# Performance work log

Hardware: AMD Instinct MI355X
Metric: run time of the kernel (lower is better)

The kernel has to match this reference:

```python
import jax, jax.numpy as jnp
import numpy as np

B, CIN, COUT, H, W = 16, 96, 96, 96, 96
K = 3   # hidden_kernels (conv), odd -> same padding
A = 3   # attn_kernels, odd -> stride-1 unfold preserves H*W positions


def _conv(x, w, p):
    # NCHW conv with symmetric padding p, stride 1, no bias
    return jax.lax.conv_general_dilated(
        x, w, window_strides=(1, 1), padding=[(p, p), (p, p)],
        dimension_numbers=("NCHW", "OIHW", "NCHW"))


def _unfold_nonoverlap(y, a):
    # torch nn.Unfold(a, stride=a): [B,C,H,W] -> [B, C*a*a, L], channel-major (c,kh,kw)
    b, c, h, w = y.shape
    hb, wb = h // a, w // a
    y = y.reshape(b, c, hb, a, wb, a).transpose(0, 1, 3, 5, 2, 4)
    return y.reshape(b, c * a * a, hb * wb)


def _unfold_stride1(y, a):
    # torch nn.Unfold(a, padding=a//2): [B,C,H,W] -> [B, C*a*a, H*W]
    b, c, h, w = y.shape
    p = a // 2
    yp = jnp.pad(y, ((0, 0), (0, 0), (p, p), (p, p)))
    # small fixed a*a loop (9 shifts), channel-major (c,kh,kw) ordering
    patches = jnp.stack([yp[:, :, i:i + h, j:j + w]
                         for i in range(a) for j in range(a)], axis=2)
    return patches.reshape(b, c * a * a, h * w)


def setup_inputs() -> dict:
    key = jax.random.key(0)
    kx, k1, k2, k3 = jax.random.split(key, 4)
    x = jax.random.normal(kx, (B, CIN, H, W), dtype=jnp.float32)
    W1 = jax.random.normal(k1, (COUT, CIN, K, K), dtype=jnp.float32) * 0.05
    W2 = jax.random.normal(k2, (COUT, CIN, K, K), dtype=jnp.float32) * 0.05
    W3 = jax.random.normal(k3, (COUT, CIN, K, K), dtype=jnp.float32) * 0.05
    return {"x": x, "W1": W1, "W2": W2, "W3": W3}


def reference(x, W1, W2, W3):
    a, c, p = A, COUT, K // 2
    b = x.shape[0]
    y1 = _unfold_nonoverlap(_conv(x, W1, p), a)   # [B, C*a^2, L]
    y2 = _unfold_nonoverlap(_conv(x, W2, p), a)   # [B, C*a^2, L]
    L = y1.shape[-1]
    y1 = y1.reshape(b, c, a * a, L).transpose(0, 2, 1, 3)  # [B, a^2, C, L]
    y2 = y2.reshape(b, c, a * a, L).transpose(0, 2, 3, 1)  # [B, a^2, L, C]
    attn = jnp.einsum("bkcl,bkld->bkcd", y1, y2)           # [B, a^2, C, C]
    # torch: transpose(1,3).flatten(2) -> [B, C, C*a^2], then scale + softmax(dim=2)
    attn = attn.transpose(0, 3, 2, 1).reshape(b, c, c * a * a)
    attn = jax.nn.softmax(attn / np.float32(np.sqrt(c * a * a)), axis=2)
    v = _unfold_stride1(_conv(x, W3, p), a)        # [B, C*a^2, H*W]
    out = jnp.einsum("bcm,bml->bcl", attn, v)      # [B, C, H*W]
    return out.reshape(b, c, H, W)
```

## Files before the change

kernel.cpp:

```cpp
#include <hip/hip_runtime.h>
#include <math.h>
#include <stdint.h>

constexpr int BB  = 16;
constexpr int CH  = 96;
constexpr int HH  = 96;
constexpr int WW  = 96;
constexpr int HWI = HH * WW;
constexpr int CHW = CH * HWI;
constexpr int IMG = BB * CHW;
constexpr int ATT = BB * CH * CH * 9;
constexpr int WPK = 27 * 6 * 64 * 8;

typedef short short8 __attribute__((ext_vector_type(8)));
typedef float floatx4 __attribute__((ext_vector_type(4)));

__device__ __forceinline__ ushort f2bf(float f) {
  union { float f; unsigned u; } v; v.f = f;
  unsigned r = (v.u + 0x7fffu + ((v.u >> 16) & 1u)) >> 16;
  return (ushort)r;
}
__device__ __forceinline__ float bf2f(ushort h) {
  union { float f; unsigned u; } v; v.u = ((unsigned)h) << 16;
  return v.f;
}
__device__ __forceinline__ uint packhl(float v) {
  const ushort h = f2bf(v);
  const ushort l = f2bf(v - bf2f(h));
  return (uint)h | ((uint)l << 16);
}

__device__ __forceinline__ void gl_lds_b128(const void* g, void* s) {
  auto gp = (const __attribute__((address_space(1))) void*)(uintptr_t)g;
  auto sp = (__attribute__((address_space(3))) void*)(uintptr_t)s;
  __builtin_amdgcn_global_load_lds(gp, sp, 16, 0, 0);
}

__global__ __launch_bounds__(256) void prepack(
    const float* __restrict__ src, ushort* __restrict__ dst)
{
  const int g = blockIdx.y;
  const int p = blockIdx.x * 256 + threadIdx.x;
  const float* s = src + (size_t)g * WPK;
  ushort* d = dst + (size_t)g * WPK;
  const int j    = p & 7;
  const int lane = (p >> 3) & 63;
  const int rest = p >> 9;
  const int mt = rest % 6;
  const int kc = rest / 6;
  const int m  = mt * 16 + (lane & 15);
  const int k  = kc * 32 + (lane >> 4) * 8 + j;
  const int ci = k % 96;
  const int o  = k / 96;
  d[p] = f2bf(s[m * 864 + ci * 9 + o]);
}

template<bool INBF, bool OUTBF>
__global__ __launch_bounds__(256, 2) void conv_mfma_t(
    const void* __restrict__ Xv, const ushort* __restrict__ Wpk,
    void* __restrict__ Yv, int wbstride)
{
  const int b    = blockIdx.y;
  const int tile = blockIdx.x;
  const int ty0  = (tile / 6) * 12;
  const int tx0  = (tile % 6) * 16;
  const int tid  = threadIdx.x;
  const int lane = tid & 63;
  const int w    = tid >> 6;
  const int nc   = lane & 15;
  const int q    = lane >> 4;

  __shared__ __attribute__((aligned(16))) ushort Xs[252 * 104];
  __shared__ __attribute__((aligned(16))) ushort Wl[2][3072];

  const ushort* wp = Wpk + (size_t)b * wbstride;

  {
    gl_lds_b128(wp + w * 512 + lane * 8,
                (ushort*)Wl[0] + __builtin_amdgcn_readfirstlane(w * 512));
    if (w < 2)
      gl_lds_b128(wp + (w + 4) * 512 + lane * 8,
                  (ushort*)Wl[0] + __builtin_amdgcn_readfirstlane((w + 4) * 512));
  }

  if (tid < 252) {
    const int ly = tid / 18, lx = tid % 18;
    const int gy = ty0 - 1 + ly, gx = tx0 - 1 + lx;
    const bool inb = ((unsigned)gy < 96u) & ((unsigned)gx < 96u);
    ushort* dst = &Xs[tid * 104];
    if constexpr (INBF) {
      const ushort* src = (const ushort*)Xv + (size_t)b * CHW + gy * WW + gx;
#pragma unroll 4
      for (int cg = 0; cg < 24; ++cg) {
        ushort u0 = 0, u1 = 0, u2 = 0, u3 = 0;
        if (inb) {
          const ushort* s = src + (size_t)(cg * 4) * HWI;
          u0 = s[0]; u1 = s[HWI]; u2 = s[2 * HWI]; u3 = s[3 * HWI];
        }
        ushort4 u; u.x = u0; u.y = u1; u.z = u2; u.w = u3;
        *(ushort4*)(dst + cg * 4) = u;
      }
    } else {
      const float* src = (const float*)Xv + (size_t)b * CHW + gy * WW + gx;
#pragma unroll 4
      for (int cg = 0; cg < 24; ++cg) {
        float f0 = 0.f, f1 = 0.f, f2 = 0.f, f3 = 0.f;
        if (inb) {
          const float* s = src + (size_t)(cg * 4) * HWI;
          f0 = s[0]; f1 = s[HWI]; f2 = s[2 * HWI]; f3 = s[3 * HWI];
        }
        ushort4 u;
        u.x = f2bf(f0); u.y = f2bf(f1); u.z = f2bf(f2); u.w = f2bf(f3);
        *(ushort4*)(dst + cg * 4) = u;
      }
    }
  }
  __syncthreads();

  floatx4 acc[6][3];
#pragma unroll
  for (int mt = 0; mt < 6; ++mt)
#pragma unroll
    for (int t = 0; t < 3; ++t)
#pragma unroll
      for (int r = 0; r < 4; ++r) acc[mt][t][r] = 0.f;

  for (int ch = 0; ch < 27; ++ch) {
    if (ch < 26) {
      const ushort* src = wp + (size_t)(ch + 1) * 3072;
      ushort* dstb = (ushort*)Wl[(ch + 1) & 1];
      gl_lds_b128(src + w * 512 + lane * 8,
                  dstb + __builtin_amdgcn_readfirstlane(w * 512));
      if (w < 2)
        gl_lds_b128(src + (w + 4) * 512 + lane * 8,
                    dstb + __builtin_amdgcn_readfirstlane((w + 4) * 512));
    }

    const ushort* wb = Wl[ch & 1];
    const int o  = ch / 3;
    const int cc = ch - o * 3;
    const int dy = o / 3, dx = o - dy * 3;
    const int pc = nc + dx;
    const int cib = cc * 32 + q * 8;

    short8 bfr[3];
#pragma unroll
    for (int t = 0; t < 3; ++t) {
      const int pix = (3 * w + t + dy) * 18 + pc;
      bfr[t] = *(const short8*)(&Xs[pix * 104 + cib]);
    }

#pragma unroll
    for (int mt = 0; mt < 6; ++mt) {
      const short8 af = *(const short8*)(wb + mt * 512 + lane * 8);
#pragma unroll
      for (int t = 0; t < 3; ++t)
        acc[mt][t] = __builtin_amdgcn_mfma_f32_16x16x32_bf16(
            af, bfr[t], acc[mt][t], 0, 0, 0);
    }
    __syncthreads();
  }

#pragma unroll
  for (int mt = 0; mt < 6; ++mt)
#pragma unroll
    for (int t = 0; t < 3; ++t) {
      const int yy = ty0 + 3 * w + t;
      const int xx = tx0 + nc;
#pragma unroll
      for (int r = 0; r < 4; ++r) {
        const int co = mt * 16 + q * 4 + r;
        const size_t off = (size_t)co * HWI + yy * WW + xx;
        if constexpr (OUTBF)
          ((ushort*)Yv + (size_t)b * CHW)[off] = f2bf(acc[mt][t][r]);
        else
          ((float*)Yv + (size_t)b * CHW)[off] = acc[mt][t][r];
      }
    }
}

__global__ __launch_bounds__(256, 2) void conv_dual_mfma(
    const float* __restrict__ X,
    const ushort* __restrict__ WpkA, const ushort* __restrict__ WpkB,
    uint* __restrict__ YA, uint* __restrict__ YB)
{
  const int b    = blockIdx.y;
  const int tile = blockIdx.x;
  const int ty0  = (tile / 6) * 12;
  const int tx0  = (tile % 6) * 16;
  const int tid  = threadIdx.x;
  const int lane = tid & 63;
  const int w    = tid >> 6;
  const int nc   = lane & 15;
  const int q    = lane >> 4;

  __shared__ __attribute__((aligned(16))) ushort Xs[252 * 104];
  __shared__ __attribute__((aligned(16))) ushort Wl[2][6144];

  {
#pragma unroll
    for (int i = 0; i < 3; ++i) {
      const int p  = w + 4 * i;
      const int cv = p / 6;
      const int pt = p - cv * 6;
      const ushort* src = (cv ? WpkB : WpkA) + pt * 512 + lane * 8;
      gl_lds_b128(src, (ushort*)Wl[0] +
                  __builtin_amdgcn_readfirstlane(cv * 3072 + pt * 512));
    }
  }

  if (tid < 252) {
    const int ly = tid / 18, lx = tid % 18;
    const int gy = ty0 - 1 + ly, gx = tx0 - 1 + lx;
    const bool inb = ((unsigned)gy < 96u) & ((unsigned)gx < 96u);
    const float* src = X + (size_t)b * CHW + gy * WW + gx;
    ushort* dst = &Xs[tid * 104];
#pragma unroll 4
    for (int cg = 0; cg < 24; ++cg) {
      float f0 = 0.f, f1 = 0.f, f2 = 0.f, f3 = 0.f;
      if (inb) {
        const float* s = src + (size_t)(cg * 4) * HWI;
        f0 = s[0]; f1 = s[HWI]; f2 = s[2 * HWI]; f3 = s[3 * HWI];
      }
      ushort4 u;
      u.x = f2bf(f0); u.y = f2bf(f1); u.z = f2bf(f2); u.w = f2bf(f3);
      *(ushort4*)(dst + cg * 4) = u;
    }
  }
  __syncthreads();

  floatx4 accA[6][3], accB[6][3];
#pragma unroll
  for (int mt = 0; mt < 6; ++mt)
#pragma unroll
    for (int t = 0; t < 3; ++t)
#pragma unroll
      for (int r = 0; r < 4; ++r) { accA[mt][t][r] = 0.f; accB[mt][t][r] = 0.f; }

  for (int ch = 0; ch < 27; ++ch) {
    if (ch < 26) {
      const size_t coff = (size_t)(ch + 1) * 3072;
      ushort* dstb = (ushort*)Wl[(ch + 1) & 1];
#pragma unroll
      for (int i = 0; i < 3; ++i) {
        const int p  = w + 4 * i;
        const int cv = p / 6;
        const int pt = p - cv * 6;
        const ushort* src = (cv ? WpkB : WpkA) + coff + pt * 512 + lane * 8;
        gl_lds_b128(src, dstb +
                    __builtin_amdgcn_readfirstlane(cv * 3072 + pt * 512));
      }
    }

    const ushort* wb = Wl[ch & 1];
    const int o  = ch / 3;
    const int cc = ch - o * 3;
    const int dy = o / 3, dx = o - dy * 3;
    const int pc = nc + dx;
    const int cib = cc * 32 + q * 8;

    short8 bfr[3];
#pragma unroll
    for (int t = 0; t < 3; ++t) {
      const int pix = (3 * w + t + dy) * 18 + pc;
      bfr[t] = *(const short8*)(&Xs[pix * 104 + cib]);
    }

#pragma unroll
    for (int mt = 0; mt < 6; ++mt) {
      const short8 afA = *(const short8*)(wb + mt * 512 + lane * 8);
#pragma unroll
      for (int t = 0; t < 3; ++t)
        accA[mt][t] = __builtin_amdgcn_mfma_f32_16x16x32_bf16(
            afA, bfr[t], accA[mt][t], 0, 0, 0);
      const short8 afB = *(const short8*)(wb + 3072 + mt * 512 + lane * 8);
#pragma unroll
      for (int t = 0; t < 3; ++t)
        accB[mt][t] = __builtin_amdgcn_mfma_f32_16x16x32_bf16(
            afB, bfr[t], accB[mt][t], 0, 0, 0);
    }
    __syncthreads();
  }

  uint* yA = YA + (size_t)b * CHW;
  uint* yB = YB + (size_t)b * CHW;
#pragma unroll
  for (int mt = 0; mt < 6; ++mt)
#pragma unroll
    for (int t = 0; t < 3; ++t) {
      const int yy = ty0 + 3 * w + t;
      const int xx = tx0 + nc;
#pragma unroll
      for (int r = 0; r < 4; ++r) {
        const int co = mt * 16 + q * 4 + r;
        yA[(size_t)co * HWI + yy * WW + xx] = packhl(accA[mt][t][r]);
        yB[(size_t)co * HWI + yy * WW + xx] = packhl(accB[mt][t][r]);
      }
    }
}

__global__ __launch_bounds__(256) void attn_mfma(
    const uint* __restrict__ Y1, const uint* __restrict__ Y2,
    float* __restrict__ P0, float* __restrict__ P1,
    float* __restrict__ P2, float* __restrict__ P3)
{
  const int bi = blockIdx.x;
  const int b  = bi / 36;
  const int r9 = bi % 36;
  const int k  = r9 >> 2;
  const int qd = r9 & 3;
  const int kh = k / 3, kw = k % 3;
  const int tid  = threadIdx.x;
  const int lane = tid & 63;
  const int wv   = tid >> 6;

  __shared__ ushort Ah[96 * 72], Al[96 * 72], Bh[96 * 72], Bl[96 * 72];

  const uint* y1b = Y1 + (size_t)b * CHW;
  const uint* y2b = Y2 + (size_t)b * CHW;

  const int mg2 = wv >> 1;
  const int ng2 = wv & 1;
  const int cn = lane & 15;
  const int q  = lane >> 4;

  floatx4 acc[3][3];
#pragma unroll
  for (int i = 0; i < 3; ++i)
#pragma unroll
    for (int j = 0; j < 3; ++j)
#pragma unroll
      for (int r = 0; r < 4; ++r) acc[i][j][r] = 0.f;

  const int sj = tid & 31;
  const int sg = tid >> 5;
  const int scol = 3 * sj + kw;

  for (int ss = 0; ss < 4; ++ss) {
    const int s = qd * 4 + ss;
    __syncthreads();
#pragma unroll
    for (int cg = 0; cg < 12; ++cg) {
      const int c = cg * 8 + sg;
      const int cbase = c * 72;
#pragma unroll
      for (int ii = 0; ii < 2; ++ii) {
        const int row = 3 * (s * 2 + ii) + kh;
        const int p   = ii * 32 + sj;
        const size_t goff = (size_t)c * HWI + row * WW + scol;
        const uint u1 = y1b[goff];
        const uint u2 = y2b[goff];
        Ah[cbase + p] = (ushort)(u1 & 0xffffu);
        Al[cbase + p] = (ushort)(u1 >> 16);
        Bh[cbase + p] = (ushort)(u2 & 0xffffu);
        Bl[cbase + p] = (ushort)(u2 >> 16);
      }
    }
    __syncthreads();

#pragma unroll
    for (int kc = 0; kc < 2; ++kc) {
      short8 ah[3], al[3], bh[3], bl[3];
#pragma unroll
      for (int t = 0; t < 3; ++t) {
        const int offA = (mg2 * 48 + t * 16 + cn) * 72 + kc * 32 + q * 8;
        ah[t] = *(const short8*)(&Ah[offA]);
        al[t] = *(const short8*)(&Al[offA]);
        const int offB = (ng2 * 48 + t * 16 + cn) * 72 + kc * 32 + q * 8;
        bh[t] = *(const short8*)(&Bh[offB]);
        bl[t] = *(const short8*)(&Bl[offB]);
      }
#pragma unroll
      for (int i = 0; i < 3; ++i)
#pragma unroll
        for (int j = 0; j < 3; ++j) {
          acc[i][j] = __builtin_amdgcn_mfma_f32_16x16x32_bf16(
              ah[i], bh[j], acc[i][j], 0, 0, 0);
          acc[i][j] = __builtin_amdgcn_mfma_f32_16x16x32_bf16(
              ah[i], bl[j], acc[i][j], 0, 0, 0);
          acc[i][j] = __builtin_amdgcn_mfma_f32_16x16x32_bf16(
              al[i], bh[j], acc[i][j], 0, 0, 0);
        }
    }
  }

  float* P = (qd == 0) ? P0 : (qd == 1) ? P1 : (qd == 2) ? P2 : P3;
#pragma unroll
  for (int i = 0; i < 3; ++i)
#pragma unroll
    for (int j = 0; j < 3; ++j)
#pragma unroll
      for (int r = 0; r < 4; ++r) {
        const int c = mg2 * 48 + i * 16 + q * 4 + r;
        const int d = ng2 * 48 + j * 16 + cn;
        P[((size_t)(b * CH + d) * CH + c) * 9 + k] = acc[i][j][r];
      }
}

__global__ __launch_bounds__(256) void softmax_k(
    const float* __restrict__ P0, const float* __restrict__ P1,
    const float* __restrict__ P2, const float* __restrict__ P3,
    float* __restrict__ attnW)
{
  const int bd = blockIdx.x;
  const size_t base = (size_t)bd * 864;
  float* dst = attnW + base;
  const float rs = 0.0340216824f;
  const int tid = threadIdx.x;

  const size_t i0 = base + tid;
  float v0 = P0[i0] + P1[i0] + P2[i0] + P3[i0];
  float v1 = P0[i0 + 256] + P1[i0 + 256] + P2[i0 + 256] + P3[i0 + 256];
  float v2 = P0[i0 + 512] + P1[i0 + 512] + P2[i0 + 512] + P3[i0 + 512];
  float v3 = (tid < 96)
      ? (P0[i0 + 768] + P1[i0 + 768] + P2[i0 + 768] + P3[i0 + 768])
      : -3.0e38f;

  float mx = fmaxf(fmaxf(v0, v1), fmaxf(v2, v3));

  __shared__ float red[256];
  red[tid] = mx;
  __syncthreads();
#pragma unroll
  for (int s = 128; s > 0; s >>= 1) {
    if (tid < s) red[tid] = fmaxf(red[tid], red[tid + s]);
    __syncthreads();
  }
  mx = red[0];
  __syncthreads();

  const float e0 = expf((v0 - mx) * rs);
  const float e1 = expf((v1 - mx) * rs);
  const float e2 = expf((v2 - mx) * rs);
  const float e3 = (tid < 96) ? expf((v3 - mx) * rs) : 0.f;

  red[tid] = e0 + e1 + e2 + e3;
  __syncthreads();
#pragma unroll
  for (int s = 128; s > 0; s >>= 1) {
    if (tid < s) red[tid] += red[tid + s];
    __syncthreads();
  }
  const float inv = 1.f / red[0];

  dst[tid]       = e0 * inv;
  dst[tid + 256] = e1 * inv;
  dst[tid + 512] = e2 * inv;
  if (tid < 96) dst[tid + 768] = e3 * inv;
}

extern "C" void kernel_launch(void* const* d_in, const int* in_sizes, int n_in,
                              void* d_out, int out_size, void* d_ws, size_t ws_size,
                              hipStream_t stream)
{
  const float* x  = (const float*)d_in[0];
  const float* W1 = (const float*)d_in[1];
  const float* W2 = (const float*)d_in[2];
  const float* W3 = (const float*)d_in[3];

  float* ws    = (float*)d_ws;
  uint*  Y1    = (uint*)ws;
  uint*  Y2    = (uint*)(ws + (size_t)IMG);
  float* attnT = ws + 2 * (size_t)IMG;
  float* attnW = attnT + ATT;
  ushort* pk   = (ushort*)(ws + 2 * (size_t)IMG + 2 * (size_t)ATT);
  ushort* pkW1 = pk;
  ushort* pkW2 = pk + WPK;
  ushort* pkW3 = pk + 2 * (size_t)WPK;
  ushort* pkAW = pk + 3 * (size_t)WPK;
  float* Pd2   = (float*)d_out;
  float* Pd3   = Pd2 + ATT;
  ushort* Y3bf = (ushort*)ws;

  const dim3 cgrid(48, BB);

  prepack  <<<dim3(324, 1),  256, 0, stream>>>(W1, pkW1);
  prepack  <<<dim3(324, 1),  256, 0, stream>>>(W2, pkW2);
  prepack  <<<dim3(324, 1),  256, 0, stream>>>(W3, pkW3);

  conv_dual_mfma<<<cgrid, 256, 0, stream>>>(x, pkW1, pkW2, Y1, Y2);

  attn_mfma<<<BB * 9 * 4, 256, 0, stream>>>(Y1, Y2, attnT, attnW, Pd2, Pd3);
  softmax_k<<<BB * CH, 256, 0, stream>>>(attnT, attnW, Pd2, Pd3, attnW);

  prepack  <<<dim3(324, BB), 256, 0, stream>>>(attnW, pkAW);

  conv_mfma_t<false, true><<<cgrid, 256, 0, stream>>>(x, pkW3, Y3bf, 0);
  conv_mfma_t<true, false><<<cgrid, 256, 0, stream>>>(Y3bf, pkAW, d_out, WPK);
}
```

Baseline: 399.6 us.

## Convert input to channel-last bf16 once and stage weights in large LDS chunks

Adds a pre-pass that casts x to bf16 in pixel-major, channel-contiguous layout, so each conv tile loads its halo with 16-byte vector loads instead of strided scalar fp32 loads. The conv kernel now stages nine weight chunks at a time in LDS (three refills, blocking) instead of double-buffering one chunk per step, which cuts barrier count but raises LDS use and limits occupancy to one block. The fused dual conv is split into two single-conv launches, and the intermediate Y3 is written channel-last for the final conv. The trade-off is an extra cast kernel and extra global traffic for the bf16 copy, lost overlap of weight loads with compute, and re-reading the input for each conv.

```diff
diff --git a/kernel.cpp b/kernel.cpp
--- a/kernel.cpp
+++ b/kernel.cpp
@@ -34,6 +34,33 @@
   auto gp = (const __attribute__((address_space(1))) void*)(uintptr_t)g;
   auto sp = (__attribute__((address_space(3))) void*)(uintptr_t)s;
   __builtin_amdgcn_global_load_lds(gp, sp, 16, 0, 0);
+}
+
+__global__ __launch_bounds__(256) void xcast(
+    const float* __restrict__ X, ushort* __restrict__ Xn)
+{
+  const int b  = blockIdx.y;
+  const int p0 = blockIdx.x * 256;
+  const int tid = threadIdx.x;
+  __shared__ ushort T[256 * 104];
+
+  const float* xb = X + (size_t)b * CHW + p0;
+#pragma unroll 8
+  for (int c = 0; c < 96; c += 2) {
+    const ushort h0 = f2bf(xb[(size_t)c * HWI + tid]);
+    const ushort h1 = f2bf(xb[(size_t)(c + 1) * HWI + tid]);
+    *(uint*)(&T[tid * 104 + c]) = (uint)h0 | ((uint)h1 << 16);
+  }
+  __syncthreads();
+
+  ushort* ob = Xn + (size_t)b * CHW + (size_t)p0 * 96;
+#pragma unroll
+  for (int it = 0; it < 12; ++it) {
+    const int idx = it * 256 + tid;
+    const int pix = (idx * 2731) >> 15;
+    const int c8  = idx - pix * 12;
+    *(short8*)(ob + pix * 96 + c8 * 8) = *(const short8*)(&T[pix * 104 + c8 * 8]);
+  }
 }
 
 __global__ __launch_bounds__(256) void prepack(
@@ -55,9 +82,10 @@
   d[p] = f2bf(s[m * 864 + ci * 9 + o]);
 }
 
-template<bool INBF, bool OUTBF>
-__global__ __launch_bounds__(256, 2) void conv_mfma_t(
-    const void* __restrict__ Xv, const ushort* __restrict__ Wpk,
+template<int OUTM>
+__global__ __launch_bounds__(256, 1) void conv_nb(
+    const ushort* __restrict__ Xn,
+    const ushort* __restrict__ Wpk,
     void* __restrict__ Yv, int wbstride)
 {
   const int b    = blockIdx.y;
@@ -71,94 +99,80 @@
   const int q    = lane >> 4;
 
   __shared__ __attribute__((aligned(16))) ushort Xs[252 * 104];
-  __shared__ __attribute__((aligned(16))) ushort Wl[2][3072];
+  __shared__ __attribute__((aligned(16))) ushort Ws[9 * 3072];
 
   const ushort* wp = Wpk + (size_t)b * wbstride;
 
-  {
-    gl_lds_b128(wp + w * 512 + lane * 8,
-                (ushort*)Wl[0] + __builtin_amdgcn_readfirstlane(w * 512));
-    if (w < 2)
-      gl_lds_b128(wp + (w + 4) * 512 + lane * 8,
-                  (ushort*)Wl[0] + __builtin_amdgcn_readfirstlane((w + 4) * 512));
-  }
-
-  if (tid < 252) {
-    const int ly = tid / 18, lx = tid % 18;
-    const int gy = ty0 - 1 + ly, gx = tx0 - 1 + lx;
-    const bool inb = ((unsigned)gy < 96u) & ((unsigned)gx < 96u);
-    ushort* dst = &Xs[tid * 104];
-    if constexpr (INBF) {
-      const ushort* src = (const ushort*)Xv + (size_t)b * CHW + gy * WW + gx;
-#pragma unroll 4
-      for (int cg = 0; cg < 24; ++cg) {
-        ushort u0 = 0, u1 = 0, u2 = 0, u3 = 0;
-        if (inb) {
-          const ushort* s = src + (size_t)(cg * 4) * HWI;
-          u0 = s[0]; u1 = s[HWI]; u2 = s[2 * HWI]; u3 = s[3 * HWI];
+  for (int i = 0; i < 14; ++i) {
+    const int pp = w + 4 * i;
+    if (pp < 54)
+      gl_lds_b128(wp + (size_t)pp * 512 + lane * 8,
+                  (ushort*)Ws + __builtin_amdgcn_readfirstlane(pp * 512));
+  }
+
+  const ushort* xb = Xn + (size_t)b * CHW;
+  for (int it = 0; it < 12; ++it) {
+    const int idx = it * 256 + tid;
+    if (idx < 3024) {
+      const int pix = (idx * 2731) >> 15;
+      const int c8  = idx - pix * 12;
+      const int ly  = (pix * 57) >> 10;
+      const int lx  = pix - ly * 18;
+      const int gy  = ty0 - 1 + ly, gx = tx0 - 1 + lx;
+      short8 v = {0, 0, 0, 0, 0, 0, 0, 0};
+      if (((unsigned)gy < 96u) & ((unsigned)gx < 96u))
+        v = *(const short8*)(xb + ((size_t)gy * WW + gx) * 96 + c8 * 8);
+      *(short8*)(&Xs[pix * 104 + c8 * 8]) = v;
+    }
+  }
+  __syncthreads();
+
+  floatx4 acc[6][3];
+#pragma unroll
+  for (int mt = 0; mt < 6; ++mt)
+#pragma unroll
+    for (int t = 0; t < 3; ++t)
+#pragma unroll
+      for (int r = 0; r < 4; ++r) acc[mt][t][r] = 0.f;
+
+  for (int g = 0; g < 3; ++g) {
+    if (g) {
+      __syncthreads();
+      for (int i = 0; i < 14; ++i) {
+        const int pp = w + 4 * i;
+        if (pp < 54)
+          gl_lds_b128(wp + (size_t)(g * 54 + pp) * 512 + lane * 8,
+                      (ushort*)Ws + __builtin_amdgcn_readfirstlane(pp * 512));
+      }
+      __syncthreads();
+    }
+
+#pragma unroll
+    for (int oo = 0; oo < 3; ++oo) {
+#pragma unroll
+      for (int cc = 0; cc < 3; ++cc) {
+        const int kcL = oo * 3 + cc;
+        const int pc  = nc + oo;
+        const int cib = cc * 32 + q * 8;
+
+        short8 bfr[3];
+#pragma unroll
+        for (int t = 0; t < 3; ++t) {
+          const int pix = (3 * w + t + g) * 18 + pc;
+          bfr[t] = *(const short8*)(&Xs[pix * 104 + cib]);
         }
-        ushort4 u; u.x = u0; u.y = u1; u.z = u2; u.w = u3;
-        *(ushort4*)(dst + cg * 4) = u;
-      }
-    } else {
-      const float* src = (const float*)Xv + (size_t)b * CHW + gy * WW + gx;
-#pragma unroll 4
-      for (int cg = 0; cg < 24; ++cg) {
-        float f0 = 0.f, f1 = 0.f, f2 = 0.f, f3 = 0.f;
-        if (inb) {
-          const float* s = src + (size_t)(cg * 4) * HWI;
-          f0 = s[0]; f1 = s[HWI]; f2 = s[2 * HWI]; f3 = s[3 * HWI];
+
+        const ushort* ap = (const ushort*)Ws + kcL * 3072 + lane * 8;
+#pragma unroll
+        for (int mt = 0; mt < 6; ++mt) {
+          const short8 af = *(const short8*)(ap + mt * 512);
+#pragma unroll
+          for (int t = 0; t < 3; ++t)
+            acc[mt][t] = __builtin_amdgcn_mfma_f32_16x16x32_bf16(
+                af, bfr[t], acc[mt][t], 0, 0, 0);
         }
-        ushort4 u;
-        u.x = f2bf(f0); u.y = f2bf(f1); u.z = f2bf(f2); u.w = f2bf(f3);
-        *(ushort4*)(dst + cg * 4) = u;
-      }
-    }
-  }
-  __syncthreads();
-
-  floatx4 acc[6][3];
-#pragma unroll
-  for (int mt = 0; mt < 6; ++mt)
-#pragma unroll
-    for (int t = 0; t < 3; ++t)
-#pragma unroll
-      for (int r = 0; r < 4; ++r) acc[mt][t][r] = 0.f;
-
-  for (int ch = 0; ch < 27; ++ch) {
-    if (ch < 26) {
-      const ushort* src = wp + (size_t)(ch + 1) * 3072;
-      ushort* dstb = (ushort*)Wl[(ch + 1) & 1];
-      gl_lds_b128(src + w * 512 + lane * 8,
-                  dstb + __builtin_amdgcn_readfirstlane(w * 512));
-      if (w < 2)
-        gl_lds_b128(src + (w + 4) * 512 + lane * 8,
-                    dstb + __builtin_amdgcn_readfirstlane((w + 4) * 512));
-    }
-
-    const ushort* wb = Wl[ch & 1];
-    const int o  = ch / 3;
-    const int cc = ch - o * 3;
-    const int dy = o / 3, dx = o - dy * 3;
-    const int pc = nc + dx;
-    const int cib = cc * 32 + q * 8;
-
-    short8 bfr[3];
-#pragma unroll
-    for (int t = 0; t < 3; ++t) {
-      const int pix = (3 * w + t + dy) * 18 + pc;
-      bfr[t] = *(const short8*)(&Xs[pix * 104 + cib]);
-    }
-
-#pragma unroll
-    for (int mt = 0; mt < 6; ++mt) {
-      const short8 af = *(const short8*)(wb + mt * 512 + lane * 8);
-#pragma unroll
-      for (int t = 0; t < 3; ++t)
-        acc[mt][t] = __builtin_amdgcn_mfma_f32_16x16x32_bf16(
-            af, bfr[t], acc[mt][t], 0, 0, 0);
-    }
-    __syncthreads();
+      }
+    }
   }
 
 #pragma unroll
@@ -170,131 +184,16 @@
 #pragma unroll
       for (int r = 0; r < 4; ++r) {
         const int co = mt * 16 + q * 4 + r;
-        const size_t off = (size_t)co * HWI + yy * WW + xx;
-        if constexpr (OUTBF)
-          ((ushort*)Yv + (size_t)b * CHW)[off] = f2bf(acc[mt][t][r]);
-        else
-          ((float*)Yv + (size_t)b * CHW)[off] = acc[mt][t][r];
-      }
-    }
-}
-
-__global__ __launch_bounds__(256, 2) void conv_dual_mfma(
-    const float* __restrict__ X,
-    const ushort* __restrict__ WpkA, const ushort* __restrict__ WpkB,
-    uint* __restrict__ YA, uint* __restrict__ YB)
-{
-  const int b    = blockIdx.y;
-  const int tile = blockIdx.x;
-  const int ty0  = (tile / 6) * 12;
-  const int tx0  = (tile % 6) * 16;
-  const int tid  = threadIdx.x;
-  const int lane = tid & 63;
-  const int w    = tid >> 6;
-  const int nc   = lane & 15;
-  const int q    = lane >> 4;
-
-  __shared__ __attribute__((aligned(16))) ushort Xs[252 * 104];
-  __shared__ __attribute__((aligned(16))) ushort Wl[2][6144];
-
-  {
-#pragma unroll
-    for (int i = 0; i < 3; ++i) {
-      const int p  = w + 4 * i;
-      const int cv = p / 6;
-      const int pt = p - cv * 6;
-      const ushort* src = (cv ? WpkB : WpkA) + pt * 512 + lane * 8;
-      gl_lds_b128(src, (ushort*)Wl[0] +
-                  __builtin_amdgcn_readfirstlane(cv * 3072 + pt * 512));
-    }
-  }
-
-  if (tid < 252) {
-    const int ly = tid / 18, lx = tid % 18;
-    const int gy = ty0 - 1 + ly, gx = tx0 - 1 + lx;
-    const bool inb = ((unsigned)gy < 96u) & ((unsigned)gx < 96u);
-    const float* src = X + (size_t)b * CHW + gy * WW + gx;
-    ushort* dst = &Xs[tid * 104];
-#pragma unroll 4
-    for (int cg = 0; cg < 24; ++cg) {
-      float f0 = 0.f, f1 = 0.f, f2 = 0.f, f3 = 0.f;
-      if (inb) {
-        const float* s = src + (size_t)(cg * 4) * HWI;
-        f0 = s[0]; f1 = s[HWI]; f2 = s[2 * HWI]; f3 = s[3 * HWI];
-      }
-      ushort4 u;
-      u.x = f2bf(f0); u.y = f2bf(f1); u.z = f2bf(f2); u.w = f2bf(f3);
-      *(ushort4*)(dst + cg * 4) = u;
-    }
-  }
-  __syncthreads();
-
-  floatx4 accA[6][3], accB[6][3];
-#pragma unroll
-  for (int mt = 0; mt < 6; ++mt)
-#pragma unroll
-    for (int t = 0; t < 3; ++t)
-#pragma unroll
-      for (int r = 0; r < 4; ++r) { accA[mt][t][r] = 0.f; accB[mt][t][r] = 0.f; }
-
-  for (int ch = 0; ch < 27; ++ch) {
-    if (ch < 26) {
-      const size_t coff = (size_t)(ch + 1) * 3072;
-      ushort* dstb = (ushort*)Wl[(ch + 1) & 1];
-#pragma unroll
-      for (int i = 0; i < 3; ++i) {
-        const int p  = w + 4 * i;
-        const int cv = p / 6;
-        const int pt = p - cv * 6;
-        const ushort* src = (cv ? WpkB : WpkA) + coff + pt * 512 + lane * 8;
-        gl_lds_b128(src, dstb +
-                    __builtin_amdgcn_readfirstlane(cv * 3072 + pt * 512));
-      }
-    }
-
-    const ushort* wb = Wl[ch & 1];
-    const int o  = ch / 3;
-    const int cc = ch - o * 3;
-    const int dy = o / 3, dx = o - dy * 3;
-    const int pc = nc + dx;
-    const int cib = cc * 32 + q * 8;
-
-    short8 bfr[3];
-#pragma unroll
-    for (int t = 0; t < 3; ++t) {
-      const int pix = (3 * w + t + dy) * 18 + pc;
-      bfr[t] = *(const short8*)(&Xs[pix * 104 + cib]);
-    }
-
-#pragma unroll
-    for (int mt = 0; mt < 6; ++mt) {
-      const short8 afA = *(const short8*)(wb + mt * 512 + lane * 8);
-#pragma unroll
-      for (int t = 0; t < 3; ++t)
-        accA[mt][t] = __builtin_amdgcn_mfma_f32_16x16x32_bf16(
-            afA, bfr[t], accA[mt][t], 0, 0, 0);
-      const short8 afB = *(const short8*)(wb + 3072 + mt * 512 + lane * 8);
-#pragma unroll
-      for (int t = 0; t < 3; ++t)
-        accB[mt][t] = __builtin_amdgcn_mfma_f32_16x16x32_bf16(
-            afB, bfr[t], accB[mt][t], 0, 0, 0);
-    }
-    __syncthreads();
-  }
-
-  uint* yA = YA + (size_t)b * CHW;
-  uint* yB = YB + (size_t)b * CHW;
-#pragma unroll
-  for (int mt = 0; mt < 6; ++mt)
-#pragma unroll
-    for (int t = 0; t < 3; ++t) {
-      const int yy = ty0 + 3 * w + t;
-      const int xx = tx0 + nc;
-#pragma unroll
-      for (int r = 0; r < 4; ++r) {
-        const int co = mt * 16 + q * 4 + r;
-        yA[(size_t)co * HWI + yy * WW + xx] = packhl(accA[mt][t][r]);
-        yB[(size_t)co * HWI + yy * WW + xx] = packhl(accB[mt][t][r]);
+        if constexpr (OUTM == 0) {
+          ((uint*)Yv + (size_t)b * CHW)[(size_t)co * HWI + yy * WW + xx] =
+              packhl(acc[mt][t][r]);
+        } else if constexpr (OUTM == 1) {
+          ((ushort*)Yv + (size_t)b * CHW)[((size_t)yy * WW + xx) * 96 + co] =
+              f2bf(acc[mt][t][r]);
+        } else {
+          ((float*)Yv + (size_t)b * CHW)[(size_t)co * HWI + yy * WW + xx] =
+              acc[mt][t][r];
+        }
       }
     }
 }
@@ -460,31 +359,35 @@
 
   float* ws    = (float*)d_ws;
   uint*  Y1    = (uint*)ws;
-  uint*  Y2    = (uint*)(ws + (size_t)IMG);
-  float* attnT = ws + 2 * (size_t)IMG;
+  uint*  Y2    = Y1 + (size_t)IMG;
+  float* attnT = (float*)(Y2 + (size_t)IMG);
   float* attnW = attnT + ATT;
-  ushort* pk   = (ushort*)(ws + 2 * (size_t)IMG + 2 * (size_t)ATT);
+  ushort* pk   = (ushort*)(attnW + ATT);
   ushort* pkW1 = pk;
   ushort* pkW2 = pk + WPK;
   ushort* pkW3 = pk + 2 * (size_t)WPK;
   ushort* pkAW = pk + 3 * (size_t)WPK;
+  ushort* Xn   = pkAW + 16 * (size_t)WPK;
   float* Pd2   = (float*)d_out;
   float* Pd3   = Pd2 + ATT;
-  ushort* Y3bf = (ushort*)ws;
+  ushort* Y3n  = (ushort*)Y1;
 
   const dim3 cgrid(48, BB);
+
+  xcast    <<<dim3(36, BB), 256, 0, stream>>>(x, Xn);
 
   prepack  <<<dim3(324, 1),  256, 0, stream>>>(W1, pkW1);
   prepack  <<<dim3(324, 1),  256, 0, stream>>>(W2, pkW2);
   prepack  <<<dim3(324, 1),  256, 0, stream>>>(W3, pkW3);
 
-  conv_dual_mfma<<<cgrid, 256, 0, stream>>>(x, pkW1, pkW2, Y1, Y2);
+  conv_nb<0><<<cgrid, 256, 0, stream>>>(Xn, pkW1, Y1, 0);
+  conv_nb<0><<<cgrid, 256, 0, stream>>>(Xn, pkW2, Y2, 0);
 
   attn_mfma<<<BB * 9 * 4, 256, 0, stream>>>(Y1, Y2, attnT, attnW, Pd2, Pd3);
   softmax_k<<<BB * CH, 256, 0, stream>>>(attnT, attnW, Pd2, Pd3, attnW);
 
   prepack  <<<dim3(324, BB), 256, 0, stream>>>(attnW, pkAW);
 
-  conv_mfma_t<false, true><<<cgrid, 256, 0, stream>>>(x, pkW3, Y3bf, 0);
-  conv_mfma_t<true, false><<<cgrid, 256, 0, stream>>>(Y3bf, pkAW, d_out, WPK);
-}
+  conv_nb<1><<<cgrid, 256, 0, stream>>>(Xn, pkW3, Y3n, 0);
+  conv_nb<2><<<cgrid, 256, 0, stream>>>(Y3n, pkAW, d_out, WPK);
+}
```

Result: faster. 391.5 us (-2.0%).
